# Optimization experiments

Hardware: AMD Instinct MI355X
Metric: run time of the kernel (lower is better)

The kernel has to match this reference:

```python
import jax, jax.numpy as jnp
import numpy as np

# Shapes hard-coded by the original module
B, C1, C2, S, K, H, E = 128, 128, 14, 14, 3, 256, 2  # batch, chan-split, chan-split, spatial, kernel, hidden, expand


def setup_inputs() -> dict:
    key = jax.random.key(0)
    k1, k2, k3 = jax.random.split(key, 3)
    x = jax.random.normal(k1, (B, C1 * C2, S), dtype=jnp.float32)
    w0 = jax.random.normal(k2, (H, E), dtype=jnp.float32)        # weights[0]
    w1 = jax.random.normal(k3, (C1, K, H), dtype=jnp.float32)    # weights[1]
    return {"x": x, "w0": w0, "w1": w1, "shift": 1}


def reference(x, w0, w1, shift):
    # reshape to (B, C1, C2, S); original torch treats it as (B, 1792, 14, 1)
    xr = x.reshape(B, C1, C2, S)
    # unfold((3,1), padding=(1,0)): 1D im2col along the S (=14) axis
    xp = jnp.pad(xr, ((0, 0), (0, 0), (0, 0), (1, 1)))
    # patches[b, j, n, i, m] = xp[b, j, n, m + i]  -> (B, C1, C2, K, S)
    patches = jnp.stack([xp[..., k:k + S] for k in range(K)], axis=3)
    # einsum 'ljnmi,jik->lnmk' (torch had m,i swapped via permute; fold it in)
    t4 = jnp.einsum('ljnim,jik->lnmk', patches, w1)   # (B, C2, S, H)
    # einsum 'kmlj,ji->kmlji': outer product with w0 along a new expand dim
    t5 = t4[..., None] * w0                            # (B, C2, S, H, E)
    t5 = jnp.roll(t5, shift, axis=1)                   # cyclic shift over C2
    t6 = jnp.transpose(t5, (0, 2, 3, 1, 4)).reshape(B, S, H, C2 * E)
    t6 = jnp.roll(t6, shift, axis=3)                   # cyclic shift over merged (C2*E)
    t6 = t6.reshape(B, S, H, C2, E).sum(axis=4)        # (B, S, H, C2)
    return jnp.transpose(t6, (0, 2, 3, 1))             # (B, H, C2, S) = (128, 256, 14, 14)
```

## Files before the change

kernel.cpp:

```cpp
#include <hip/hip_runtime.h>
#include <hip/hip_bf16.h>
#include <math.h>

#define B_   128
#define C1_  128
#define C2_  14
#define S_   14
#define K_   3
#define H_   256
#define E_   2

#define HT   64
#define NT   4
#define XROWS 224
#define XSTR 72
#define BSTR 200
#define CROW 228

typedef unsigned short u16;
typedef unsigned int   u32;
typedef __attribute__((ext_vector_type(8))) short bf16x8;
typedef __attribute__((ext_vector_type(4))) float f32x4;

__device__ __forceinline__ u16 f2bf(float f) {
    u32 u = __float_as_uint(f);
    return (u16)((u + 0x7FFF + ((u >> 16) & 1)) >> 16);
}

__device__ __forceinline__ int decode_shift(const int* p) {
    int a = p[0];
    if (a >= -100 && a <= 100 && a != 0) return a;
    float f = __int_as_float(a);
    if (f >= -100.f && f <= 100.f && f == truncf(f) && f != 0.f) return (int)f;
    long long bits = ((long long)p[1] << 32) | (unsigned int)a;
    double d = __longlong_as_double(bits);
    if (d >= -100.0 && d <= 100.0 && d == trunc(d) && d != 0.0) return (int)d;
    return a;
}

__global__ __launch_bounds__(256) void cvt_kernel(const float* __restrict__ x,
                                                  const float* __restrict__ w1,
                                                  u16* __restrict__ xg,
                                                  u16* __restrict__ wg) {
    const int blk = blockIdx.x;
    if (blk < 256) {
        __shared__ u16 xl[64 * 200];
        const int b = blk >> 1, hf = blk & 1;
        const float4* src = (const float4*)(x + (size_t)(b * C1_ + hf * 64) * 196);
        for (int q = threadIdx.x; q < 12544; q += 256) {
            float4 v = src[q];
            int c1l = q / 49, f4 = q - c1l * 49;
            uint2 w;
            w.x = (u32)f2bf(v.x) | ((u32)f2bf(v.y) << 16);
            w.y = (u32)f2bf(v.z) | ((u32)f2bf(v.w) << 16);
            *(uint2*)&xl[c1l * 200 + f4 * 4] = w;
        }
        __syncthreads();
        u16* dst = xg + (size_t)(b * 2 + hf) * (XROWS * 64);
        for (int idx = threadIdx.x; idx < 1792; idx += 256) {
            int row = idx >> 3, o = idx & 7;
            int c2 = row >> 4, p = row & 15;
            uint4 val = make_uint4(0, 0, 0, 0);
            if (p >= 1 && p <= 14) {
                int cs = c2 * 14 + p - 1;
                u16 v[8];
#pragma unroll
                for (int j = 0; j < 8; ++j) v[j] = xl[(o * 8 + j) * 200 + cs];
                val.x = (u32)v[0] | ((u32)v[1] << 16);
                val.y = (u32)v[2] | ((u32)v[3] << 16);
                val.z = (u32)v[4] | ((u32)v[5] << 16);
                val.w = (u32)v[6] | ((u32)v[7] << 16);
            }
            *(uint4*)&dst[idx * 8] = val;
        }
    } else {
        const int base = (blk - 256) * 1536;
        for (int ii = threadIdx.x; ii < 1536; ii += 256) {
            int idx = base + ii;
            int co = idx % 24;
            int rest = idx / 24;
            int hl = rest & 63;
            int g2 = rest >> 6;
            int hf = g2 & 1, g = g2 >> 1;
            int kk = co >> 3, c1o = co & 7;
            u16 v[8];
#pragma unroll
            for (int j = 0; j < 8; ++j) {
                int c1 = hf * 64 + c1o * 8 + j;
                v[j] = f2bf(w1[((size_t)c1 * K_ + kk) * H_ + g * 64 + hl]);
            }
            uint4 val;
            val.x = (u32)v[0] | ((u32)v[1] << 16);
            val.y = (u32)v[2] | ((u32)v[3] << 16);
            val.z = (u32)v[4] | ((u32)v[5] << 16);
            val.w = (u32)v[6] | ((u32)v[7] << 16);
            *(uint4*)&wg[(size_t)idx * 8] = val;
        }
    }
}

__global__ __launch_bounds__(256, 2) void fused_kernel(const u16* __restrict__ xg,
                                                       const float* __restrict__ w0,
                                                       const u16* __restrict__ wg,
                                                       const int* __restrict__ shift_p,
                                                       float* __restrict__ out) {
    __shared__ __align__(16) char lds[58368];
    u16*   xT = (u16*)lds;
    u16*   Bt = (u16*)(lds + 32544);
    float* Cl = (float*)lds;

    const int b    = blockIdx.x >> 2;
    const int g    = blockIdx.x & 3;
    const int h0   = g * HT;
    const int t    = threadIdx.x;
    const int wave = t >> 6;
    const int lane = t & 63;
    const int quad = lane >> 4;
    const int l15  = lane & 15;

    f32x4 acc[4][NT];
#pragma unroll
    for (int i = 0; i < 4; ++i)
#pragma unroll
        for (int j = 0; j < NT; ++j) acc[i][j] = (f32x4){0.f, 0.f, 0.f, 0.f};

    for (int hf = 0; hf < 2; ++hf) {
        if (hf) __syncthreads();
        {
            const uint4* src = (const uint4*)(xg + (size_t)(b * 2 + hf) * (XROWS * 64));
#pragma unroll
            for (int i = 0; i < 7; ++i) {
                int idx = t + 256 * i;
                uint4 v = src[idx];
                *(uint4*)&xT[(idx >> 3) * XSTR + (idx & 7) * 8] = v;
            }
        }
        {
            const uint4* src = (const uint4*)(wg + (size_t)(g * 2 + hf) * (64 * 192));
#pragma unroll
            for (int i = 0; i < 6; ++i) {
                int idx = t + 256 * i;
                uint4 v = src[idx];
                int hl = idx / 24, co = idx - hl * 24;
                *(uint4*)&Bt[hl * BSTR + co * 8] = v;
            }
        }
        __syncthreads();

#pragma unroll
        for (int tt = 0; tt < 6; ++tt) {
            const int kk = tt >> 1;
            const int coff = (tt & 1) * 32 + quad * 8;
            bf16x8 bfr[NT];
#pragma unroll
            for (int nc = 0; nc < NT; ++nc)
                bfr[nc] = *(const bf16x8*)&Bt[(nc * 16 + l15) * BSTR + kk * 64 + coff];
#pragma unroll
            for (int mi = 0; mi < 4; ++mi) {
                int mt = wave + mi * 4;
                if (mt < 14) {
                    int r = mt * 16 + l15;
                    bf16x8 af = *(const bf16x8*)&xT[(r + kk) * XSTR + coff];
#pragma unroll
                    for (int nc = 0; nc < NT; ++nc)
                        acc[mi][nc] = __builtin_amdgcn_mfma_f32_16x16x32_bf16(
                            af, bfr[nc], acc[mi][nc], 0, 0, 0);
                }
            }
        }
    }

    __syncthreads();
#pragma unroll
    for (int mi = 0; mi < 4; ++mi) {
        int mt = wave + mi * 4;
        if (mt < 14) {
#pragma unroll
            for (int nc = 0; nc < NT; ++nc) {
                int hl = nc * 16 + l15;
                *(f32x4*)&Cl[hl * CROW + mt * 16 + quad * 4] = acc[mi][nc];
            }
        }
    }
    __syncthreads();

    const int shift = decode_shift(shift_p);
    const int hl = t >> 2, sub = t & 3;
    const int h = h0 + hl;
    int c0[2]; float wv[2];
#pragma unroll
    for (int e = 0; e < 2; ++e) {
        int q = (e - shift) % 28; if (q < 0) q += 28;
        int np0 = q >> 1, ep = q & 1;
        int c = (np0 - shift) % 14; if (c < 0) c += 14;
        c0[e] = c;
        wv[e] = w0[h * 2 + ep];
    }
    const float* Crow = &Cl[hl * CROW];
    float* orow = out + (size_t)(b * H_ + h) * 196;
#pragma unroll
    for (int jj = 0; jj < 13; ++jj) {
        int i = sub + 4 * jj;
        if (i < 49) {
            float tmp[4];
#pragma unroll
            for (int e4 = 0; e4 < 4; ++e4) {
                int idx = 4 * i + e4;
                int n = idx / 14, m = idx - n * 14;
                int cA = c0[0] + n; if (cA >= 14) cA -= 14;
                int cB = c0[1] + n; if (cB >= 14) cB -= 14;
                tmp[e4] = wv[0] * Crow[cA * 16 + m] + wv[1] * Crow[cB * 16 + m];
            }
            *(float4*)&orow[4 * i] = make_float4(tmp[0], tmp[1], tmp[2], tmp[3]);
        }
    }
}

__global__ __launch_bounds__(256) void t4_fb(const float* __restrict__ x,
                                             const float* __restrict__ w1,
                                             float* __restrict__ t4) {
    __shared__ float xl[C1_][16];
    const int b = blockIdx.x / C2_, c2 = blockIdx.x % C2_, h = threadIdx.x;
    for (int i = h; i < C1_ * S_; i += 256) {
        int c1 = i / S_, s = i % S_;
        xl[c1][s + 1] = x[((size_t)(b * C1_ + c1) * C2_ + c2) * S_ + s];
    }
    if (h < C1_) { xl[h][0] = 0.f; xl[h][15] = 0.f; }
    __syncthreads();
    float acc[S_];
#pragma unroll
    for (int s = 0; s < S_; ++s) acc[s] = 0.f;
    for (int c1 = 0; c1 < C1_; ++c1) {
        float wa = w1[(size_t)(c1 * K_ + 0) * H_ + h];
        float wb = w1[(size_t)(c1 * K_ + 1) * H_ + h];
        float wc = w1[(size_t)(c1 * K_ + 2) * H_ + h];
#pragma unroll
        for (int s = 0; s < S_; ++s)
            acc[s] += wa * xl[c1][s] + wb * xl[c1][s + 1] + wc * xl[c1][s + 2];
    }
    size_t base = ((size_t)(b * H_ + h) * C2_ + c2) * S_;
#pragma unroll
    for (int s = 0; s < S_; ++s) t4[base + s] = acc[s];
}
__global__ __launch_bounds__(224) void out_fb(float* __restrict__ t4,
                                              const float* __restrict__ w0,
                                              const int* __restrict__ shift_p) {
    const int tid = threadIdx.x;
    const int m = tid % S_, hh = tid / S_;
    const int b = blockIdx.x / 16, h = (blockIdx.x % 16) * 16 + hh;
    const int shift = decode_shift(shift_p);
    const size_t colbase = ((size_t)(b * H_ + h) * C2_) * S_ + m;
    float tl[C2_];
#pragma unroll
    for (int c2 = 0; c2 < C2_; ++c2) tl[c2] = t4[colbase + (size_t)c2 * S_];
    const float w0v[2] = { w0[h * 2 + 0], w0[h * 2 + 1] };
    float r[C2_];
#pragma unroll
    for (int n = 0; n < C2_; ++n) {
        float a = 0.f;
#pragma unroll
        for (int e = 0; e < 2; ++e) {
            int q = (2 * n + e - shift) % 28; if (q < 0) q += 28;
            int np = q >> 1, ep = q & 1;
            int c2 = (np - shift) % 14; if (c2 < 0) c2 += 14;
            a += tl[c2] * w0v[ep];
        }
        r[n] = a;
    }
#pragma unroll
    for (int n = 0; n < C2_; ++n) t4[colbase + (size_t)n * S_] = r[n];
}

extern "C" void kernel_launch(void* const* d_in, const int* in_sizes, int n_in,
                              void* d_out, int out_size, void* d_ws, size_t ws_size,
                              hipStream_t stream) {
    const float* x     = (const float*)d_in[0];
    const float* w0    = (const float*)d_in[1];
    const float* w1    = (const float*)d_in[2];
    const int*   shift = (const int*)(n_in > 3 ? d_in[3] : d_in[n_in - 1]);
    for (int i = 0; i < n_in; ++i) {
        int sz = in_sizes[i];
        if (sz == B_ * C1_ * C2_ * S_)      x     = (const float*)d_in[i];
        else if (sz == H_ * E_)             w0    = (const float*)d_in[i];
        else if (sz == C1_ * K_ * H_)       w1    = (const float*)d_in[i];
        else if (sz == 1)                   shift = (const int*)d_in[i];
    }
    float* out = (float*)d_out;

    const size_t NXG = (size_t)B_ * 2 * XROWS * 64;
    const size_t NWG = (size_t)4 * 2 * 64 * 192;
    if (ws_size >= (NXG + NWG) * sizeof(u16)) {
        u16* xg = (u16*)d_ws;
        u16* wg = xg + NXG;
        cvt_kernel<<<264, 256, 0, stream>>>(x, w1, xg, wg);
        fused_kernel<<<B_ * 4, 256, 0, stream>>>(xg, w0, wg, shift, out);
    } else {
        t4_fb<<<B_ * C2_, 256, 0, stream>>>(x, w1, out);
        out_fb<<<B_ * 16, 224, 0, stream>>>(out, w0, shift);
    }
}
```

Before: 105.4 us.

## Split conversion pre-pass into finer blocks and coalesce weight reads

The x-to-bf16 transpose pre-pass now uses four blocks per (batch, half) pair, each covering a quarter of the spatial columns, so 1024 blocks are launched instead of 256 and each needs a much smaller shared-memory tile. The weight conversion now reads w1 with coalesced float4 loads and scatters 2-byte stores, replacing the earlier strided scalar gathers. The aim is more parallelism and better-latency hiding in the pre-pass. In exchange the x loads become scalar rather than float4, and the weight stores become scattered narrow writes.

New measurement: 89.91 us. 1.17x faster.

```diff
diff --git a/kernel.cpp b/kernel.cpp
--- a/kernel.cpp
+++ b/kernel.cpp
@@ -43,58 +43,58 @@
                                                   u16* __restrict__ xg,
                                                   u16* __restrict__ wg) {
     const int blk = blockIdx.x;
-    if (blk < 256) {
-        __shared__ u16 xl[64 * 200];
-        const int b = blk >> 1, hf = blk & 1;
-        const float4* src = (const float4*)(x + (size_t)(b * C1_ + hf * 64) * 196);
-        for (int q = threadIdx.x; q < 12544; q += 256) {
-            float4 v = src[q];
-            int c1l = q / 49, f4 = q - c1l * 49;
-            uint2 w;
-            w.x = (u32)f2bf(v.x) | ((u32)f2bf(v.y) << 16);
-            w.y = (u32)f2bf(v.z) | ((u32)f2bf(v.w) << 16);
-            *(uint2*)&xl[c1l * 200 + f4 * 4] = w;
+    const int t   = threadIdx.x;
+    if (blk < 1024) {
+        __shared__ u16 xl[64 * 50];
+        const int b   = blk >> 3;
+        const int hf  = (blk >> 2) & 1;
+        const int qr  = blk & 3;
+        const int cs0 = qr * 49;
+        const float* xb = x + (size_t)(b * C1_ + hf * 64) * 196 + cs0;
+#pragma unroll
+        for (int i = 0; i < 13; ++i) {
+            int idx = t + 256 * i;
+            if (idx < 3136) {
+                int c1l = idx / 49, j = idx - c1l * 49;
+                xl[c1l * 50 + j] = f2bf(xb[c1l * 196 + j]);
+            }
         }
         __syncthreads();
-        u16* dst = xg + (size_t)(b * 2 + hf) * (XROWS * 64);
-        for (int idx = threadIdx.x; idx < 1792; idx += 256) {
-            int row = idx >> 3, o = idx & 7;
-            int c2 = row >> 4, p = row & 15;
-            uint4 val = make_uint4(0, 0, 0, 0);
-            if (p >= 1 && p <= 14) {
-                int cs = c2 * 14 + p - 1;
-                u16 v[8];
-#pragma unroll
-                for (int j = 0; j < 8; ++j) v[j] = xl[(o * 8 + j) * 200 + cs];
-                val.x = (u32)v[0] | ((u32)v[1] << 16);
-                val.y = (u32)v[2] | ((u32)v[3] << 16);
-                val.z = (u32)v[4] | ((u32)v[5] << 16);
-                val.w = (u32)v[6] | ((u32)v[7] << 16);
-            }
-            *(uint4*)&dst[idx * 8] = val;
+        u16* dst = xg + ((size_t)(b * 2 + hf) * XROWS + qr * 56) * 64;
+#pragma unroll
+        for (int i = 0; i < 2; ++i) {
+            int task = t + 256 * i;
+            if (task < 448) {
+                int rr = task >> 3, o = task & 7;
+                int row = qr * 56 + rr;
+                int p = row & 15;
+                uint4 val = make_uint4(0, 0, 0, 0);
+                if (p >= 1 && p <= 14) {
+                    int csl = (row >> 4) * 14 + p - 1 - cs0;
+                    u16 v[8];
+#pragma unroll
+                    for (int j = 0; j < 8; ++j) v[j] = xl[(o * 8 + j) * 50 + csl];
+                    val.x = (u32)v[0] | ((u32)v[1] << 16);
+                    val.y = (u32)v[2] | ((u32)v[3] << 16);
+                    val.z = (u32)v[4] | ((u32)v[5] << 16);
+                    val.w = (u32)v[6] | ((u32)v[7] << 16);
+                }
+                *(uint4*)&dst[(size_t)rr * 64 + o * 8] = val;
+            }
         }
     } else {
-        const int base = (blk - 256) * 1536;
-        for (int ii = threadIdx.x; ii < 1536; ii += 256) {
-            int idx = base + ii;
-            int co = idx % 24;
-            int rest = idx / 24;
-            int hl = rest & 63;
-            int g2 = rest >> 6;
-            int hf = g2 & 1, g = g2 >> 1;
-            int kk = co >> 3, c1o = co & 7;
-            u16 v[8];
-#pragma unroll
-            for (int j = 0; j < 8; ++j) {
-                int c1 = hf * 64 + c1o * 8 + j;
-                v[j] = f2bf(w1[((size_t)c1 * K_ + kk) * H_ + g * 64 + hl]);
-            }
-            uint4 val;
-            val.x = (u32)v[0] | ((u32)v[1] << 16);
-            val.y = (u32)v[2] | ((u32)v[3] << 16);
-            val.z = (u32)v[4] | ((u32)v[5] << 16);
-            val.w = (u32)v[6] | ((u32)v[7] << 16);
-            *(uint4*)&wg[(size_t)idx * 8] = val;
+        int q = (blk - 1024) * 256 + t;
+        float4 v = ((const float4*)w1)[q];
+        int i0 = q * 4;
+        int c1 = i0 / 768;
+        int kk = (i0 - c1 * 768) >> 8;
+        int h0 = i0 & 255;
+        int hf = c1 >> 6, c1l = c1 & 63;
+        u16 b4[4] = { f2bf(v.x), f2bf(v.y), f2bf(v.z), f2bf(v.w) };
+#pragma unroll
+        for (int d = 0; d < 4; ++d) {
+            int h = h0 + d, g = h >> 6, hl = h & 63;
+            wg[(size_t)((g * 2 + hf) * 64 + hl) * 192 + kk * 64 + c1l] = b4[d];
         }
     }
 }
@@ -292,7 +292,7 @@
     if (ws_size >= (NXG + NWG) * sizeof(u16)) {
         u16* xg = (u16*)d_ws;
         u16* wg = xg + NXG;
-        cvt_kernel<<<264, 256, 0, stream>>>(x, w1, xg, wg);
+        cvt_kernel<<<1024 + 96, 256, 0, stream>>>(x, w1, xg, wg);
         fused_kernel<<<B_ * 4, 256, 0, stream>>>(xg, w0, wg, shift, out);
     } else {
         t4_fb<<<B_ * C2_, 256, 0, stream>>>(x, w1, out);
```
